# Optimization experiments

Measured on AMD Instinct MI355X. Metric: run time of the kernel, lower is better.

## Reference

```python
import jax, jax.numpy as jnp
import numpy as np

NUM_EMBEDDINGS = 4096
EMBED_DIM = 256
BETA = 0.25


def setup_inputs() -> dict:
    key = jax.random.key(0)
    kz, ke = jax.random.split(key)
    z = jax.random.normal(kz, (16, 4096, EMBED_DIM), dtype=jnp.float32)
    lim = 1.0 / NUM_EMBEDDINGS
    emb = jax.random.uniform(ke, (NUM_EMBEDDINGS, EMBED_DIM), dtype=jnp.float32,
                             minval=-lim, maxval=lim)
    return {"z": z, "emb": emb}


def reference(z, emb):
    B, T, D = z.shape
    flat_z = z.reshape(-1, D)                                  # [N, D]
    # squared euclidean distances via ||z||^2 - 2 z.e^T + ||e||^2
    dist = (jnp.sum(flat_z ** 2, axis=1, keepdims=True)
            - 2.0 * flat_z @ emb.T
            + jnp.sum(emb ** 2, axis=1))                       # [N, K]
    indices = jnp.argmin(dist, axis=1)                         # [N]
    z_q = emb[indices].reshape(z.shape)                        # [B, T, D]
    sg = jax.lax.stop_gradient
    codebook_loss = jnp.mean((sg(z_q) - z) ** 2)
    commit_loss = jnp.mean((z_q - sg(z)) ** 2)
    loss = codebook_loss + BETA * commit_loss
    z_q_st = z + sg(z_q - z)                                   # straight-through
    return z_q_st, loss, indices.reshape(B, T)
```

## Files before the change

kernel.cpp:

```cpp
#include <hip/hip_runtime.h>

#define N_ROWS 65536
#define K_CODES 4096
#define D_DIM 256
#define MARGIN_BF 6.0e-5f
#define CAP_DUEL 24576
#define CAP_FULL 8192

typedef __attribute__((ext_vector_type(8))) _Float16 f16x8;
typedef __attribute__((ext_vector_type(4))) float f32x4;


union f16u { _Float16 h; unsigned short u; };

static __device__ __forceinline__ unsigned int pack2(float a, float b) {
    f16u x, y; x.h = (_Float16)a; y.h = (_Float16)b;
    return (unsigned)x.u | ((unsigned)y.u << 16);
}

static __device__ __forceinline__ void norm_body(const float* __restrict__ src,
                                                 float* __restrict__ dst, int bi, int tid) {
    int row = bi * 64 + (tid >> 2);
    int q = tid & 3;
    const float* p = src + (size_t)row * D_DIM;
    double acc = 0.0;
#pragma unroll 4
    for (int it = 0; it < 16; ++it) {
        float4 v = *(const float4*)&p[(q + 4 * it) * 4];
        float a = v.x * v.x, b = v.y * v.y, c = v.z * v.z, d = v.w * v.w;
        acc += (double)a; acc += (double)b; acc += (double)c; acc += (double)d;
    }
    acc += __shfl_xor(acc, 1);
    acc += __shfl_xor(acc, 2);
    if (q == 0) dst[row] = (float)acc;
}

__global__ __launch_bounds__(256) void cvt_emb_kernel(const float* __restrict__ emb,
                                                      unsigned short* __restrict__ emb_perm,
                                                      float* __restrict__ cvec,
                                                      int* __restrict__ cnts) {
    if (blockIdx.x >= 512) {
        if (blockIdx.x == 512 && threadIdx.x < 2) cnts[threadIdx.x] = 0;
        norm_body(emb, cvec, blockIdx.x - 512, threadIdx.x);
        return;
    }
    int gid = blockIdx.x * 256 + threadIdx.x;
    int lane = gid & 63;
    int f = gid >> 6;
    int cf = f & 1;
    int d8 = (f >> 1) & 7;
    int step = (f >> 4) & 63;
    int h = f >> 10;
    int code = h * 2048 + step * 32 + cf * 16 + (lane & 15);
    int d0 = d8 * 32 + (lane >> 4) * 8;
    const float* p = emb + (size_t)code * D_DIM + d0;
    float4 v0 = *(const float4*)p;
    float4 v1 = *(const float4*)(p + 4);
    uint4 o;
    o.x = pack2(v0.x * 4096.0f, v0.y * 4096.0f);
    o.y = pack2(v0.z * 4096.0f, v0.w * 4096.0f);
    o.z = pack2(v1.x * 4096.0f, v1.y * 4096.0f);
    o.w = pack2(v1.z * 4096.0f, v1.w * 4096.0f);
    *(uint4*)((char*)emb_perm + (size_t)gid * 16) = o;
}

__global__ __launch_bounds__(256) void cvt_z_kernel(const float* __restrict__ z,
                                                    unsigned short* __restrict__ z_perm,
                                                    float* __restrict__ rownorm,
                                                    unsigned long long* __restrict__ rescored) {
    if (blockIdx.x >= 8192) {
        norm_body(z, rownorm, blockIdx.x - 8192, threadIdx.x);
        return;
    }
    if (blockIdx.x < 256) rescored[blockIdx.x * 256 + threadIdx.x] = ~0ull;
    int ft = blockIdx.x * 256 + threadIdx.x;
    int lane = ft & 63;
    int rf = (ft >> 6) & 3;
    int d8 = (ft >> 8) & 7;
    int rg = ft >> 11;
    int row = rg * 64 + rf * 16 + (lane & 15);
    int d0 = d8 * 32 + (lane >> 4) * 8;
    const float* p = z + (size_t)row * D_DIM + d0;
    float4 v0 = *(const float4*)p;
    float4 v1 = *(const float4*)(p + 4);
    uint4 o;
    o.x = pack2(v0.x, v0.y);
    o.y = pack2(v0.z, v0.w);
    o.z = pack2(v1.x, v1.y);
    o.w = pack2(v1.z, v1.w);
    *(uint4*)((char*)z_perm + (size_t)ft * 16) = o;
}

__global__ __launch_bounds__(256, 2) void phaseB_kernel(
        const unsigned short* __restrict__ z_perm, const unsigned short* __restrict__ emb_perm,
        const float* __restrict__ cvec, float* __restrict__ out_idx,
        int* __restrict__ cnts, int* __restrict__ fulllist,
        unsigned long long* __restrict__ duellist) {
    __shared__ float cv[4096];

    const int tid = threadIdx.x;
    const int lane = tid & 63;
    const int w = tid >> 6;
    const int pp = w >> 1;
    const int h = w & 1;
    const int l15 = lane & 15, l4 = lane >> 4;
    const int rb = blockIdx.x;

#pragma unroll
    for (int i = 0; i < 4; ++i) {
        int idx = i * 1024 + tid * 4;
        *(float4*)&cv[idx] = *(const float4*)&cvec[idx];
    }

    f16x8 A[8][4];
    {
        const char* zsrc = (const char*)z_perm + (size_t)(rb * 2 + pp) * 32768 + lane * 16;
#pragma unroll
        for (int d8 = 0; d8 < 8; ++d8)
#pragma unroll
            for (int rf = 0; rf < 4; ++rf)
                A[d8][rf] = *(const f16x8*)(zsrc + (d8 * 4 + rf) * 1024);
    }
    __syncthreads();

    const char* bq = (const char*)emb_perm + (size_t)h * 1048576 + lane * 16;
    f16x8 Ra0, Rb0, Ra1, Rb1, Ra2, Rb2, Ra3, Rb3;
    Ra0 = *(const f16x8*)(bq);        Rb0 = *(const f16x8*)(bq + 1024);
    Ra1 = *(const f16x8*)(bq + 2048); Rb1 = *(const f16x8*)(bq + 3072);
    Ra2 = *(const f16x8*)(bq + 4096); Rb2 = *(const f16x8*)(bq + 5120);

    float m1[16], m2[16], m3[16];
#pragma unroll
    for (int t = 0; t < 16; ++t) { m1[t] = 3.4e38f; m2[t] = 3.4e38f; m3[t] = 3.4e38f; }

    f32x4 acc[4][2];

    for (int step = 0; step < 64; ++step) {
        const int kb = h * 2048 + step * 32;
        float ck0 = cv[kb + l15];
        float ck1 = cv[kb + 16 + l15];
#pragma unroll
        for (int rf = 0; rf < 4; ++rf) {
            acc[rf][0] = (f32x4){0.f, 0.f, 0.f, 0.f};
            acc[rf][1] = (f32x4){0.f, 0.f, 0.f, 0.f};
        }
#pragma unroll
        for (int d8 = 0; d8 < 8; ++d8) {
            const char* pf = bq + (d8 + 3) * 2048;
            switch ((d8 + 3) & 3) {
                case 0: Ra0 = *(const f16x8*)pf; Rb0 = *(const f16x8*)(pf + 1024); break;
                case 1: Ra1 = *(const f16x8*)pf; Rb1 = *(const f16x8*)(pf + 1024); break;
                case 2: Ra2 = *(const f16x8*)pf; Rb2 = *(const f16x8*)(pf + 1024); break;
                default: Ra3 = *(const f16x8*)pf; Rb3 = *(const f16x8*)(pf + 1024); break;
            }
            f16x8 b0, b1;
            switch (d8 & 3) {
                case 0: b0 = Ra0; b1 = Rb0; break;
                case 1: b0 = Ra1; b1 = Rb1; break;
                case 2: b0 = Ra2; b1 = Rb2; break;
                default: b0 = Ra3; b1 = Rb3; break;
            }
#pragma unroll
            for (int rf = 0; rf < 4; ++rf) {
                acc[rf][0] = __builtin_amdgcn_mfma_f32_16x16x32_f16(A[d8][rf], b0, acc[rf][0], 0, 0, 0);
                acc[rf][1] = __builtin_amdgcn_mfma_f32_16x16x32_f16(A[d8][rf], b1, acc[rf][1], 0, 0, 0);
            }
        }
        bq += 16384;

#pragma unroll
        for (int cf = 0; cf < 2; ++cf) {
            const float ck = cf ? ck1 : ck0;
            const unsigned cg = (unsigned)(kb + cf * 16 + l15);
#pragma unroll
            for (int rf = 0; rf < 4; ++rf)
#pragma unroll
                for (int j = 0; j < 4; ++j) {
                    float d = fmaf(-4.8828125e-4f, acc[rf][cf][j], ck);
                    float dp = __uint_as_float((__float_as_uint(d) & 0xfffff000u) | cg);
                    const int t = rf * 4 + j;
                    m3[t] = __builtin_amdgcn_fmed3f(dp, m2[t], m3[t]);
                    m2[t] = __builtin_amdgcn_fmed3f(dp, m1[t], m2[t]);
                    m1[t] = fminf(m1[t], dp);
                }
        }
    }

    __syncthreads();
    float* m1s = cv;
    float* m2s = cv + 256;
    float* m3s = cv + 512;
#pragma unroll
    for (int t = 0; t < 16; ++t) {
        float a1 = m1[t], a2 = m2[t], a3 = m3[t];
        for (int msk = 8; msk >= 1; msk >>= 1) {
            float b1 = __shfl_xor(a1, msk);
            float b2 = __shfl_xor(a2, msk);
            float b3 = __shfl_xor(a3, msk);
            bool bw = b1 < a1;
            float w1 = bw ? b1 : a1, w2 = bw ? b2 : a2, w3 = bw ? b3 : a3;
            float l1 = bw ? a1 : b1, l2 = bw ? a2 : b2;
            bool t2 = l1 < w2;
            a1 = w1;
            a2 = t2 ? l1 : w2;
            a3 = t2 ? fminf(w2, l2) : fminf(w3, l1);
        }
        if (l15 == 0) {
            int rloc = (t >> 2) * 16 + l4 * 4 + (t & 3);
            m1s[w * 64 + rloc] = a1;
            m2s[w * 64 + rloc] = a2;
            m3s[w * 64 + rloc] = a3;
        }
    }
    __syncthreads();

    if (tid < 128) {
        int pg = tid >> 6, r = tid & 63;
        int wA = pg * 2, wB = pg * 2 + 1;
        float a1 = m1s[wA * 64 + r], a2 = m2s[wA * 64 + r], a3 = m3s[wA * 64 + r];
        float b1 = m1s[wB * 64 + r], b2 = m2s[wB * 64 + r], b3 = m3s[wB * 64 + r];
        bool bw = b1 < a1;
        float w1 = bw ? b1 : a1, w2 = bw ? b2 : a2, w3 = bw ? b3 : a3;
        float l1 = bw ? a1 : b1, l2 = bw ? a2 : b2;
        bool t2 = l1 < w2;
        float f1 = w1;
        float f2 = t2 ? l1 : w2;
        float f3 = t2 ? fminf(w2, l2) : fminf(w3, l1);

        int i1 = (int)(__float_as_uint(f1) & 0xfffu);
        int i2 = (int)(__float_as_uint(f2) & 0xfffu);
        int rowg = rb * 128 + pg * 64 + r;
        out_idx[rowg] = (float)i1;
        if (f3 - f1 < MARGIN_BF) {
            int pz = atomicAdd(&cnts[1], 1);
            if (pz < CAP_FULL) fulllist[pz] = rowg;
        } else if (f2 - f1 < MARGIN_BF) {
            int pz = atomicAdd(&cnts[0], 1);
            if (pz < CAP_DUEL) {
                duellist[pz] = ((unsigned long long)(unsigned)rowg << 32) |
                               ((unsigned)i1 << 16) | (unsigned)i2;
            } else {
                int pf = atomicAdd(&cnts[1], 1);
                if (pf < CAP_FULL) fulllist[pf] = rowg;
            }
        }
    }
}

__global__ __launch_bounds__(256) void duel_kernel(
        const float* __restrict__ z, const float* __restrict__ emb,
        const float* __restrict__ rownorm, const float* __restrict__ cvec,
        const int* __restrict__ cnts, const unsigned long long* __restrict__ duellist,
        unsigned long long* __restrict__ rescored) {
    int n = cnts[0];
    if (n > CAP_DUEL) n = CAP_DUEL;
    for (int i = blockIdx.x * 256 + threadIdx.x; i < n; i += 64 * 256) {
        unsigned long long e = duellist[i];
        int row = (int)(e >> 32);
        int c1 = (int)((e >> 16) & 0xfffu);
        int c2 = (int)(e & 0xfffu);
        const float* zp = z + (size_t)row * D_DIM;
        const float* p1 = emb + (size_t)c1 * D_DIM;
        const float* p2 = emb + (size_t)c2 * D_DIM;
        float a1 = 0.f, a2 = 0.f;
#pragma unroll 8
        for (int d4 = 0; d4 < 64; ++d4) {
            float4 zf = *(const float4*)&zp[d4 * 4];
            float4 e1 = *(const float4*)&p1[d4 * 4];
            float4 e2 = *(const float4*)&p2[d4 * 4];
            a1 = fmaf(zf.x, e1.x, a1); a1 = fmaf(zf.y, e1.y, a1);
            a1 = fmaf(zf.z, e1.z, a1); a1 = fmaf(zf.w, e1.w, a1);
            a2 = fmaf(zf.x, e2.x, a2); a2 = fmaf(zf.y, e2.y, a2);
            a2 = fmaf(zf.z, e2.z, a2); a2 = fmaf(zf.w, e2.w, a2);
        }
        float rn = rownorm[row];
        float d1 = __fadd_rn(__fsub_rn(rn, __fmul_rn(2.0f, a1)), cvec[c1]);
        float d2 = __fadd_rn(__fsub_rn(rn, __fmul_rn(2.0f, a2)), cvec[c2]);
        unsigned long long p1v = ((unsigned long long)__float_as_uint(d1) << 32) | (unsigned)c1;
        unsigned long long p2v = ((unsigned long long)__float_as_uint(d2) << 32) | (unsigned)c2;
        rescored[row] = p1v < p2v ? p1v : p2v;
    }
}

__global__ __launch_bounds__(256) void rescore_kernel(
        const float* __restrict__ z, const float* __restrict__ emb,
        const float* __restrict__ rownorm, const float* __restrict__ cvec,
        const int* __restrict__ cnts, const int* __restrict__ fulllist,
        unsigned long long* __restrict__ rescored) {
    __shared__ float zs[16][256];
    __shared__ float sa[16];
    __shared__ int srow[16];
    const int tid = threadIdx.x;
    int cnt = cnts[1];
    if (cnt > CAP_FULL) cnt = CAP_FULL;
    const int nu = ((cnt + 15) >> 4) << 2;
    for (int uu = blockIdx.x; uu < nu; uu += gridDim.x) {
        int rg = uu >> 2, ks = uu & 3;
        __syncthreads();
        if (tid < 16) {
            int fi = rg * 16 + tid;
            int row = fulllist[fi < cnt ? fi : 0];
            srow[tid] = row;
            sa[tid] = rownorm[row];
        }
        __syncthreads();
#pragma unroll
        for (int i = 0; i < 4; ++i) {
            int u = i * 256 + tid;
            int r = u >> 6, d4 = u & 63;
            *(float4*)&zs[r][d4 * 4] = *(const float4*)&z[(size_t)srow[r] * D_DIM + d4 * 4];
        }
        __syncthreads();

        const int c0 = ks * 1024 + tid;
        float acc[16][4];
#pragma unroll
        for (int r = 0; r < 16; ++r)
#pragma unroll
            for (int j = 0; j < 4; ++j) acc[r][j] = 0.f;

        for (int ch = 0; ch < 8; ++ch) {
#pragma unroll
            for (int q = 0; q < 8; ++q) {
                float4 e0 = *(const float4*)&emb[(size_t)(c0      ) * D_DIM + ch * 32 + q * 4];
                float4 e1 = *(const float4*)&emb[(size_t)(c0 + 256) * D_DIM + ch * 32 + q * 4];
                float4 e2 = *(const float4*)&emb[(size_t)(c0 + 512) * D_DIM + ch * 32 + q * 4];
                float4 e3 = *(const float4*)&emb[(size_t)(c0 + 768) * D_DIM + ch * 32 + q * 4];
#pragma unroll
                for (int r = 0; r < 16; ++r) {
                    float4 zf = *(const float4*)&zs[r][ch * 32 + q * 4];
                    acc[r][0] = fmaf(zf.x, e0.x, acc[r][0]);
                    acc[r][0] = fmaf(zf.y, e0.y, acc[r][0]);
                    acc[r][0] = fmaf(zf.z, e0.z, acc[r][0]);
                    acc[r][0] = fmaf(zf.w, e0.w, acc[r][0]);
                    acc[r][1] = fmaf(zf.x, e1.x, acc[r][1]);
                    acc[r][1] = fmaf(zf.y, e1.y, acc[r][1]);
                    acc[r][1] = fmaf(zf.z, e1.z, acc[r][1]);
                    acc[r][1] = fmaf(zf.w, e1.w, acc[r][1]);
                    acc[r][2] = fmaf(zf.x, e2.x, acc[r][2]);
                    acc[r][2] = fmaf(zf.y, e2.y, acc[r][2]);
                    acc[r][2] = fmaf(zf.z, e2.z, acc[r][2]);
                    acc[r][2] = fmaf(zf.w, e2.w, acc[r][2]);
                    acc[r][3] = fmaf(zf.x, e3.x, acc[r][3]);
                    acc[r][3] = fmaf(zf.y, e3.y, acc[r][3]);
                    acc[r][3] = fmaf(zf.z, e3.z, acc[r][3]);
                    acc[r][3] = fmaf(zf.w, e3.w, acc[r][3]);
                }
            }
        }
        const float ck0 = cvec[c0], ck1 = cvec[c0 + 256];
        const float ck2 = cvec[c0 + 512], ck3 = cvec[c0 + 768];
#pragma unroll
        for (int r = 0; r < 16; ++r) {
            float d0 = __fadd_rn(__fsub_rn(sa[r], __fmul_rn(2.0f, acc[r][0])), ck0);
            float d1 = __fadd_rn(__fsub_rn(sa[r], __fmul_rn(2.0f, acc[r][1])), ck1);
            float d2 = __fadd_rn(__fsub_rn(sa[r], __fmul_rn(2.0f, acc[r][2])), ck2);
            float d3 = __fadd_rn(__fsub_rn(sa[r], __fmul_rn(2.0f, acc[r][3])), ck3);
            unsigned long long p0 = ((unsigned long long)__float_as_uint(d0) << 32) | (unsigned)(c0);
            unsigned long long p1 = ((unsigned long long)__float_as_uint(d1) << 32) | (unsigned)(c0 + 256);
            unsigned long long p2 = ((unsigned long long)__float_as_uint(d2) << 32) | (unsigned)(c0 + 512);
            unsigned long long p3 = ((unsigned long long)__float_as_uint(d3) << 32) | (unsigned)(c0 + 768);
            unsigned long long pa = p0 < p1 ? p0 : p1;
            unsigned long long pb = p2 < p3 ? p2 : p3;
            unsigned long long pm = pa < pb ? pa : pb;
            for (int msk = 32; msk >= 1; msk >>= 1) {
                unsigned long long qv = __shfl_xor(pm, msk);
                pm = qv < pm ? qv : pm;
            }
            if ((tid & 63) == 0) atomicMin(&rescored[srow[r]], pm);
        }
    }
}

__global__ __launch_bounds__(256) void writeback_kernel(
        const float* __restrict__ z, const float* __restrict__ emb,
        const unsigned long long* __restrict__ rescored,
        float* __restrict__ out_idx, float* __restrict__ out0,
        double* __restrict__ partials) {
    const int tid = threadIdx.x;
    const int base = blockIdx.x * 32;
    double acc = 0.0;
    for (int g = 0; g < 8; ++g) {
        int row = base + g * 4 + (tid >> 6);
        int d4 = tid & 63;
        unsigned long long rv = rescored[row];
        int idx;
        if (rv != ~0ull) {
            idx = (int)(unsigned)(rv & 0xffffffffull);
            if (d4 == 0) out_idx[row] = (float)idx;
        } else {
            idx = (int)out_idx[row];
        }
        float4 q4 = *(const float4*)&emb[(size_t)idx * D_DIM + d4 * 4];
        float4 z4 = *(const float4*)&z[(size_t)row * D_DIM + d4 * 4];
        float4 o;
        float dx;
        dx = q4.x - z4.x; o.x = z4.x + dx; acc += (double)dx * dx;
        dx = q4.y - z4.y; o.y = z4.y + dx; acc += (double)dx * dx;
        dx = q4.z - z4.z; o.z = z4.z + dx; acc += (double)dx * dx;
        dx = q4.w - z4.w; o.w = z4.w + dx; acc += (double)dx * dx;
        *(float4*)&out0[(size_t)row * D_DIM + d4 * 4] = o;
    }
    for (int m = 32; m >= 1; m >>= 1) acc += __shfl_xor(acc, m);
    __shared__ double sd[4];
    if ((tid & 63) == 0) sd[tid >> 6] = acc;
    __syncthreads();
    if (tid == 0) partials[blockIdx.x] = (sd[0] + sd[1]) + (sd[2] + sd[3]);
}

__global__ void finalize_kernel(const double* __restrict__ partials, float* __restrict__ out_loss) {
    __shared__ double sd[256];
    const int tid = threadIdx.x;
    double a = 0.0;
    for (int i = tid; i < 2048; i += 256) a += partials[i];
    sd[tid] = a;
    __syncthreads();
    for (int s = 128; s > 0; s >>= 1) {
        if (tid < s) sd[tid] += sd[tid + s];
        __syncthreads();
    }
    if (tid == 0) {
        double m = sd[0] / 16777216.0;
        out_loss[0] = (float)(m + 0.25 * m);
    }
}

extern "C" void kernel_launch(void* const* d_in, const int* in_sizes, int n_in,
                              void* d_out, int out_size, void* d_ws, size_t ws_size,
                              hipStream_t stream) {
    const float* z = (const float*)d_in[0];
    const float* emb = (const float*)d_in[1];
    float* out0 = (float*)d_out;
    float* out_loss = out0 + (size_t)N_ROWS * D_DIM;
    float* out_idx = out_loss + 1;

    char* ws = (char*)d_ws;
    float* rownorm = (float*)ws;
    float* cvec = (float*)(ws + 262144);
    unsigned short* emb_perm = (unsigned short*)(ws + 278528);
    int* cnts = (int*)(ws + 2375680);
    int* fulllist = (int*)(ws + 2375936);
    unsigned long long* duellist = (unsigned long long*)(ws + 2408704);
    unsigned long long* rescored = (unsigned long long*)(ws + 2605312);
    double* partials = (double*)(ws + 3129600);

    unsigned short* z_perm = (unsigned short*)d_out;

    cvt_emb_kernel<<<576, 256, 0, stream>>>(emb, emb_perm, cvec, cnts);
    cvt_z_kernel<<<9216, 256, 0, stream>>>(z, z_perm, rownorm, rescored);
    phaseB_kernel<<<512, 256, 0, stream>>>(z_perm, emb_perm, cvec, out_idx, cnts, fulllist, duellist);
    rescore_kernel<<<256, 256, 0, stream>>>(z, emb, rownorm, cvec, cnts, fulllist, rescored);
    duel_kernel<<<64, 256, 0, stream>>>(z, emb, rownorm, cvec, cnts, duellist, rescored);
    writeback_kernel<<<N_ROWS / 32, 256, 0, stream>>>(z, emb, rescored, out_idx, out0, partials);
    finalize_kernel<<<1, 256, 0, stream>>>(partials, out_loss);
}
```

Before: 304.7 us.

## Stage codebook tiles through an LDS ring via global_load_lds instead of per-wave register prefetch

Replaces the per-wave direct global loads of the permuted codebook with a shared 8-slot LDS ring per half, filled by global_load_lds DMA. The two waves sharing a half each fetch half of each tile, so every codebook byte is loaded once per block from global memory rather than once per wave. Each d8 substep now carries a vmcnt wait plus a workgroup barrier before reading B operands from LDS. This adds sync overhead and LDS traffic in the hot MFMA loop, and the last steps wrap the prefetch address back to the start of the codebook.

```diff
diff --git a/kernel.cpp b/kernel.cpp
--- a/kernel.cpp
+++ b/kernel.cpp
@@ -9,6 +9,10 @@
 
 typedef __attribute__((ext_vector_type(8))) _Float16 f16x8;
 typedef __attribute__((ext_vector_type(4))) float f32x4;
+
+typedef __attribute__((address_space(1))) unsigned int g_u32;
+typedef __attribute__((address_space(3))) unsigned int l_u32;
+#define GLOAD16(gp, lp) __builtin_amdgcn_global_load_lds((g_u32*)(gp), (l_u32*)(lp), 16, 0, 0)
 
 
 union f16u { _Float16 h; unsigned short u; };
@@ -97,6 +101,7 @@
         int* __restrict__ cnts, int* __restrict__ fulllist,
         unsigned long long* __restrict__ duellist) {
     __shared__ float cv[4096];
+    __shared__ unsigned short ring[2][8][1024];
 
     const int tid = threadIdx.x;
     const int lane = tid & 63;
@@ -123,11 +128,20 @@
     }
     __syncthreads();
 
-    const char* bq = (const char*)emb_perm + (size_t)h * 1048576 + lane * 16;
-    f16x8 Ra0, Rb0, Ra1, Rb1, Ra2, Rb2, Ra3, Rb3;
-    Ra0 = *(const f16x8*)(bq);        Rb0 = *(const f16x8*)(bq + 1024);
-    Ra1 = *(const f16x8*)(bq + 2048); Rb1 = *(const f16x8*)(bq + 3072);
-    Ra2 = *(const f16x8*)(bq + 4096); Rb2 = *(const f16x8*)(bq + 5120);
+    const char* bsrc = (const char*)emb_perm + (size_t)h * 1048576 + pp * 1024 + lane * 16;
+    char* ldst = (char*)&ring[h][0][0] + pp * 1024;
+    const char* lrd = (const char*)&ring[h][0][0] + lane * 16;
+
+#pragma unroll
+    for (int q = 0; q < 6; ++q)
+        GLOAD16(bsrc + q * 2048, ldst + q * 2048);
+    asm volatile("s_waitcnt vmcnt(5)" ::: "memory");
+    __builtin_amdgcn_s_barrier();
+    __builtin_amdgcn_sched_barrier(0);
+
+    f16x8 B0a = *(const f16x8*)(lrd);
+    f16x8 B0b = *(const f16x8*)(lrd + 1024);
+    f16x8 B1a, B1b;
 
     float m1[16], m2[16], m3[16];
 #pragma unroll
@@ -146,27 +160,27 @@
         }
 #pragma unroll
         for (int d8 = 0; d8 < 8; ++d8) {
-            const char* pf = bq + (d8 + 3) * 2048;
-            switch ((d8 + 3) & 3) {
-                case 0: Ra0 = *(const f16x8*)pf; Rb0 = *(const f16x8*)(pf + 1024); break;
-                case 1: Ra1 = *(const f16x8*)pf; Rb1 = *(const f16x8*)(pf + 1024); break;
-                case 2: Ra2 = *(const f16x8*)pf; Rb2 = *(const f16x8*)(pf + 1024); break;
-                default: Ra3 = *(const f16x8*)pf; Rb3 = *(const f16x8*)(pf + 1024); break;
-            }
-            f16x8 b0, b1;
-            switch (d8 & 3) {
-                case 0: b0 = Ra0; b1 = Rb0; break;
-                case 1: b0 = Ra1; b1 = Rb1; break;
-                case 2: b0 = Ra2; b1 = Rb2; break;
-                default: b0 = Ra3; b1 = Rb3; break;
-            }
+            {
+                const char* g = bsrc + (size_t)(step * 8 + d8 + 6) * 2048
+                                - ((step == 63 && d8 >= 2) ? 1048576 : 0);
+                GLOAD16(g, ldst + ((d8 + 6) & 7) * 2048);
+            }
+            asm volatile("s_waitcnt vmcnt(5)" ::: "memory");
+            __builtin_amdgcn_s_barrier();
+            __builtin_amdgcn_sched_barrier(0);
+            {
+                const char* rp = lrd + ((d8 + 1) & 7) * 2048;
+                if ((d8 + 1) & 1) { B1a = *(const f16x8*)rp; B1b = *(const f16x8*)(rp + 1024); }
+                else              { B0a = *(const f16x8*)rp; B0b = *(const f16x8*)(rp + 1024); }
+            }
+            f16x8 b0 = (d8 & 1) ? B1a : B0a;
+            f16x8 b1 = (d8 & 1) ? B1b : B0b;
 #pragma unroll
             for (int rf = 0; rf < 4; ++rf) {
                 acc[rf][0] = __builtin_amdgcn_mfma_f32_16x16x32_f16(A[d8][rf], b0, acc[rf][0], 0, 0, 0);
                 acc[rf][1] = __builtin_amdgcn_mfma_f32_16x16x32_f16(A[d8][rf], b1, acc[rf][1], 0, 0, 0);
             }
         }
-        bq += 16384;
 
 #pragma unroll
         for (int cf = 0; cf < 2; ++cf) {
```

New measurement: 296.1 us. 1.03x faster.
